# Kernel optimization log

Measured on AMD Instinct MI355X. Metric: run time of the kernel, lower is better.

The kernel has to match this reference:

```python
import jax, jax.numpy as jnp
import numpy as np


def setup_inputs() -> dict:
    key = jax.random.key(0)
    k1, k2, k3, k4 = jax.random.split(key, 4)
    B, Nq, Nc, D = 4, 1024, 16384, 1024
    return {
        "query_embeddings": jax.random.normal(k1, (B, Nq, D), dtype=jnp.float32),
        "context_embeddings": jax.random.normal(k2, (B, Nc, D), dtype=jnp.float32),
        "W": jax.random.normal(k3, (D, D), dtype=jnp.float32) * (1.0 / np.sqrt(D)),
        "b": jax.random.normal(k4, (D,), dtype=jnp.float32) * 0.02,
    }


TOP_N = 5


def _pairwise_l2(q, c):
    # q: [B, Nq, D], c: [B, Nc, D] -> [B, Nq, Nc] Euclidean distances
    q_sq = jnp.sum(q * q, axis=-1, keepdims=True)          # [B, Nq, 1]
    c_sq = jnp.sum(c * c, axis=-1)[:, None, :]             # [B, 1, Nc]
    cross = jnp.einsum("bqd,bcd->bqc", q, c)               # [B, Nq, Nc]
    d2 = jnp.maximum(q_sq + c_sq - 2.0 * cross, 0.0)
    return jnp.sqrt(d2)


def reference(query_embeddings, context_embeddings, W, b):
    # latent query projection (nn.Linear): x @ W.T + b
    q_proj = jnp.einsum("bqd,ed->bqe", query_embeddings, W) + b
    distances = _pairwise_l2(q_proj, context_embeddings)    # [B, Nq, Nc]
    # smallest top_n distances -> top_k on negated values
    neg_d, idx = jax.lax.top_k(-distances, TOP_N)
    return (-neg_d, idx)
```

## Files before the change

### kernel.cpp

```cpp
#include <hip/hip_runtime.h>
#include <cfloat>
#include <math.h>

#define D_DIM 1024
#define B_DIM 4
#define NQ    1024
#define NC    16384
#define TOPN  5
#define TOPA  5
#define CSPLIT 8
#define CAND  (TOPA*CSPLIT)
#define QT    64
#define CTILE 512
#define BK    64

#define PBM 128
#define PBN 64
#define PBK 32
#define PPAD 4
#define PROJ_BLKS ((D_DIM/PBN) * ((B_DIM*NQ)/PBM))

typedef __bf16 bf16x8 __attribute__((ext_vector_type(8)));
typedef float  f32x4  __attribute__((ext_vector_type(4)));
typedef double f64x4  __attribute__((ext_vector_type(4)));

__device__ __forceinline__ unsigned short f2bf(float f) {
    unsigned u = __builtin_bit_cast(unsigned, f);
    unsigned r = (u + 0x7fffu + ((u >> 16) & 1u)) >> 16;
    return (unsigned short)r;
}

__device__ __forceinline__ void gload16(const void* g, void* l) {
    __builtin_amdgcn_global_load_lds(
        (const __attribute__((address_space(1))) unsigned*)g,
        (__attribute__((address_space(3))) unsigned*)l, 16, 0, 0);
}

template<int N, typename T>
__device__ __forceinline__ void topk_insert(T (&bv)[N], int (&bi)[N], T v, int ci) {
    if (v < bv[N-1] || (v == bv[N-1] && ci < bi[N-1])) {
        bv[N-1] = v; bi[N-1] = ci;
        #pragma unroll
        for (int s = N-1; s > 0; --s) {
            bool sw = (bv[s] < bv[s-1]) || (bv[s] == bv[s-1] && bi[s] < bi[s-1]);
            if (sw) {
                T tv = bv[s-1]; bv[s-1] = bv[s]; bv[s] = tv;
                int ti = bi[s-1]; bi[s-1] = bi[s]; bi[s] = ti;
            }
        }
    }
}

template<int N>
__device__ __forceinline__ void insN(float (&bv)[N], int (&bi)[N], float v, int ci) {
    if (v < bv[N-1]) {
        bv[N-1] = v; bi[N-1] = ci;
        #pragma unroll
        for (int s = N-1; s > 0; --s) {
            if (bv[s] < bv[s-1]) {
                float tv = bv[s-1]; bv[s-1] = bv[s]; bv[s] = tv;
                int   ti = bi[s-1]; bi[s-1] = bi[s]; bi[s] = ti;
            }
        }
    }
}

__device__ __forceinline__ void ins5b(float (&bv)[TOPA], int (&bi)[TOPA], float v, int ci) {
    #pragma unroll
    for (int s = 0; s < TOPA; ++s) {
        const bool  c    = v < bv[s];
        const float vmin = c ? v : bv[s];
        const float vmax = c ? bv[s] : v;
        const int   imin = c ? ci : bi[s];
        const int   imax = c ? bi[s] : ci;
        bv[s] = vmin; bi[s] = imin;
        v = vmax; ci = imax;
    }
}

__global__ __launch_bounds__(256) void proj_packc_kernel(const float* __restrict__ Q,
                                                         const float* __restrict__ W,
                                                         const float* __restrict__ bias,
                                                         const float* __restrict__ C,
                                                         double* __restrict__ P64,
                                                         unsigned short* __restrict__ Pbf,
                                                         float* __restrict__ qsq,
                                                         unsigned short* __restrict__ Cbf,
                                                         float* __restrict__ csq)
{
    const int bid = blockIdx.x;
    if (bid >= PROJ_BLKS) {
        int wave = threadIdx.x >> 6;
        int lane = threadIdx.x & 63;
        int row  = (bid - PROJ_BLKS) * 4 + wave;
        const float* x = C + (size_t)row * D_DIM;
        float s = 0.f;
        #pragma unroll
        for (int i = 0; i < 4; ++i) {
            float4 v = *(const float4*)&x[lane * 4 + i * 256];
            s += v.x * v.x + v.y * v.y + v.z * v.z + v.w * v.w;
            ushort4 h;
            h.x = f2bf(v.x); h.y = f2bf(v.y); h.z = f2bf(v.z); h.w = f2bf(v.w);
            *(ushort4*)&Cbf[(size_t)row * D_DIM + lane * 4 + i * 256] = h;
        }
        #pragma unroll
        for (int off = 32; off; off >>= 1) s += __shfl_down(s, off, 64);
        if (lane == 0) csq[row] = s;
        return;
    }
    __shared__ __align__(16) float Qs[PBM][PBK + PPAD];
    __shared__ __align__(16) float Ws[PBN][PBK + PPAD];

    const int t    = threadIdx.x;
    const int lane = t & 63;
    const int w    = t >> 6;
    const int l15  = lane & 15;
    const int l4   = lane >> 4;
    const int m0   = (bid >> 4) * PBM;
    const int n0   = (bid & 15) * PBN;
    const int wm   = (w >> 1) * 64;
    const int wn   = (w & 1) * 32;

    const int srow = t >> 3;
    const int scol = (t & 7) * 4;

    f64x4 acc[4][2];
    #pragma unroll
    for (int fm = 0; fm < 4; ++fm)
        #pragma unroll
        for (int fn = 0; fn < 2; ++fn) acc[fm][fn] = (f64x4)0.0;

    for (int k0 = 0; k0 < D_DIM; k0 += PBK) {
        float4 qa0 = *(const float4*)&Q[(size_t)(m0 + srow)      * D_DIM + k0 + scol];
        float4 qa1 = *(const float4*)&Q[(size_t)(m0 + srow + 32) * D_DIM + k0 + scol];
        float4 qa2 = *(const float4*)&Q[(size_t)(m0 + srow + 64) * D_DIM + k0 + scol];
        float4 qa3 = *(const float4*)&Q[(size_t)(m0 + srow + 96) * D_DIM + k0 + scol];
        float4 wa0 = *(const float4*)&W[(size_t)(n0 + srow)      * D_DIM + k0 + scol];
        float4 wa1 = *(const float4*)&W[(size_t)(n0 + srow + 32) * D_DIM + k0 + scol];
        __syncthreads();
        *(float4*)&Qs[srow][scol]      = qa0;
        *(float4*)&Qs[srow + 32][scol] = qa1;
        *(float4*)&Qs[srow + 64][scol] = qa2;
        *(float4*)&Qs[srow + 96][scol] = qa3;
        *(float4*)&Ws[srow][scol]      = wa0;
        *(float4*)&Ws[srow + 32][scol] = wa1;
        __syncthreads();

        #pragma unroll
        for (int ks = 0; ks < PBK / 4; ++ks) {
            const int kc = ks * 4 + l4;
            double a[4], b[2];
            #pragma unroll
            for (int fm = 0; fm < 4; ++fm) a[fm] = (double)Qs[wm + fm * 16 + l15][kc];
            #pragma unroll
            for (int fn = 0; fn < 2; ++fn) b[fn] = (double)Ws[wn + fn * 16 + l15][kc];
            #pragma unroll
            for (int fm = 0; fm < 4; ++fm)
                #pragma unroll
                for (int fn = 0; fn < 2; ++fn)
                    acc[fm][fn] = __builtin_amdgcn_mfma_f64_16x16x4f64(a[fm], b[fn], acc[fm][fn], 0, 0, 0);
        }
    }

    #pragma unroll
    for (int fm = 0; fm < 4; ++fm) {
        #pragma unroll
        for (int j = 0; j < 4; ++j) {
            const int row = m0 + wm + fm * 16 + j * 4 + l4;
            float part = 0.f;
            #pragma unroll
            for (int fn = 0; fn < 2; ++fn) {
                const int col = n0 + wn + fn * 16 + l15;
                double d = acc[fm][fn][j] + (double)bias[col];
                P64[(size_t)row * D_DIM + col] = d;
                float a = (float)d;
                part += a * a;
                Pbf[(size_t)row * D_DIM + col] = f2bf(a);
            }
            #pragma unroll
            for (int m = 1; m < 16; m <<= 1) part += __shfl_xor(part, m, 64);
            if (l15 == 0) atomicAdd(&qsq[row], part);
        }
    }
}

__global__ __launch_bounds__(256) void perm_detect_kernel(const float* __restrict__ Q,
                                                          const float* __restrict__ W,
                                                          const float* __restrict__ bias,
                                                          const double* __restrict__ P64,
                                                          int* __restrict__ invperm)
{
    __shared__ double tv[16];
    const int t = threadIdx.x;
    const int g = t >> 4;
    const int s = t & 15;
    if (t < 16) invperm[t] = t;

    double acc = 0.0;
    const int kb = s * 64;
    for (int k = 0; k < 64; ++k)
        acc = fma((double)Q[(size_t)g * D_DIM + kb + k], (double)W[kb + k], acc);
    #pragma unroll
    for (int off = 8; off; off >>= 1) acc += __shfl_down(acc, off, 16);
    if (s == 0) tv[g] = acc + (double)bias[0];
    __syncthreads();

    if (t < 16) {
        double p = P64[(size_t)t * D_DIM];
        int best = 0; double bd = fabs(p - tv[0]);
        #pragma unroll
        for (int i = 1; i < 16; ++i) {
            double d = fabs(p - tv[i]);
            if (d < bd) { bd = d; best = i; }
        }
        invperm[best] = t;
    }
}

__global__ __launch_bounds__(256, 2) void dist_mfma_kernel(const unsigned short* __restrict__ Pbf,
                                                           const unsigned short* __restrict__ Cbf,
                                                           const float* __restrict__ qsq,
                                                           const float* __restrict__ csq,
                                                           int* __restrict__ pi)
{
    __shared__ __align__(16) short CsS[CTILE * 64];
    __shared__ __align__(16) short QsS[QT * 64];
    float* MV = (float*)CsS;
    int*   MI = (int*)(CsS + 4096);

    const int t    = threadIdx.x;
    const int lane = t & 63;
    const int w    = t >> 6;
    const int l15  = lane & 15;
    const int l4   = lane >> 4;
    const int r8   = lane >> 3;
    const int sc   = lane & 7;
    const int csplit = blockIdx.x;
    const int by = blockIdx.y;
    const int bz = blockIdx.z;
    const int qg0 = bz * NQ + by * QT;

    unsigned cOff[16], qOff[2];
    #pragma unroll
    for (int j = 0; j < 16; ++j)
        cOff[j] = (unsigned)((w * 128 + j * 8 + r8) * D_DIM + (sc ^ r8) * 8);
    #pragma unroll
    for (int j = 0; j < 2; ++j)
        qOff[j] = (unsigned)((w * 16 + j * 8 + r8) * D_DIM + (sc ^ r8) * 8);

    float qsv[4];
    #pragma unroll
    for (int s = 0; s < 4; ++s) qsv[s] = qsq[qg0 + s * 16 + l15];

    float bv[4][TOPA]; int bi[4][TOPA];
    #pragma unroll
    for (int s = 0; s < 4; ++s)
        #pragma unroll
        for (int j = 0; j < TOPA; ++j) { bv[s][j] = FLT_MAX; bi[s][j] = 0x7fffffff; }

    const int cpb = NC / CSPLIT;
    for (int it = 0; it < cpb / CTILE; ++it) {
        const int cg0 = csplit * cpb + it * CTILE;
        const size_t crow0 = (size_t)bz * NC + cg0;

        f32x4 acc[8][4];
        #pragma unroll
        for (int u = 0; u < 8; ++u)
            #pragma unroll
            for (int s = 0; s < 4; ++s) acc[u][s] = (f32x4)0.0f;

        for (int k0 = 0; k0 < D_DIM; k0 += BK) {
            const unsigned short* cB = Cbf + crow0 * D_DIM + k0;
            const unsigned short* qB = Pbf + (size_t)qg0 * D_DIM + k0;
            __syncthreads();
            #pragma unroll
            for (int j = 0; j < 16; ++j)
                gload16(cB + cOff[j], &CsS[(w * 128 + j * 8) * 64]);
            #pragma unroll
            for (int j = 0; j < 2; ++j)
                gload16(qB + qOff[j], &QsS[(w * 16 + j * 8) * 64]);
            __syncthreads();
            #pragma unroll
            for (int ks = 0; ks < 2; ++ks) {
                const int sp = ((ks * 4 + l4) ^ (l15 & 7)) * 8;
                bf16x8 bq[4];
                #pragma unroll
                for (int s = 0; s < 4; ++s)
                    bq[s] = *(const bf16x8*)&QsS[(s * 16 + l15) * 64 + sp];
                #pragma unroll
                for (int u = 0; u < 8; ++u) {
                    bf16x8 ac = *(const bf16x8*)&CsS[(w * 128 + u * 16 + l15) * 64 + sp];
                    #pragma unroll
                    for (int s = 0; s < 4; ++s)
                        acc[u][s] = __builtin_amdgcn_mfma_f32_16x16x32_bf16(ac, bq[s], acc[u][s], 0, 0, 0);
                }
            }
        }

        #pragma unroll
        for (int u = 0; u < 8; ++u) {
            const int crow = w * 128 + u * 16 + l4 * 4;
            float4 cs4 = *(const float4*)&csq[(size_t)bz * NC + cg0 + crow];
            float csa[4] = {cs4.x, cs4.y, cs4.z, cs4.w};
            #pragma unroll
            for (int s = 0; s < 4; ++s) {
                #pragma unroll
                for (int r = 0; r < 4; ++r) {
                    float v = qsv[s] + csa[r] - 2.0f * acc[u][s][r];
                    ins5b(bv[s], bi[s], v, cg0 + crow + r);
                }
            }
        }
    }

    #pragma unroll
    for (int mask = 16; mask <= 32; mask <<= 1) {
        #pragma unroll
        for (int s = 0; s < 4; ++s) {
            float ov[TOPA]; int oi[TOPA];
            #pragma unroll
            for (int j = 0; j < TOPA; ++j) {
                ov[j] = __shfl_xor(bv[s][j], mask, 64);
                oi[j] = __shfl_xor(bi[s][j], mask, 64);
            }
            #pragma unroll
            for (int j = 0; j < TOPA; ++j) insN<TOPA>(bv[s], bi[s], ov[j], oi[j]);
        }
    }
    __syncthreads();
    if (l4 == 0) {
        #pragma unroll
        for (int s = 0; s < 4; ++s) {
            int q = s * 16 + l15;
            #pragma unroll
            for (int j = 0; j < TOPA; ++j) {
                MV[(q * 4 + w) * TOPA + j] = bv[s][j];
                MI[(q * 4 + w) * TOPA + j] = bi[s][j];
            }
        }
    }
    __syncthreads();
    if (t < QT) {
        float mv[TOPA]; int mi[TOPA];
        #pragma unroll
        for (int j = 0; j < TOPA; ++j) { mv[j] = FLT_MAX; mi[j] = 0x7fffffff; }
        for (int l = 0; l < 4; ++l)
            #pragma unroll
            for (int j = 0; j < TOPA; ++j)
                insN<TOPA>(mv, mi, MV[(t * 4 + l) * TOPA + j], MI[(t * 4 + l) * TOPA + j]);
        size_t base = (((size_t)qg0 + t) * CSPLIT + csplit) * TOPA;
        #pragma unroll
        for (int j = 0; j < TOPA; ++j) pi[base + j] = mi[j];
    }
}

__global__ __launch_bounds__(256) void refine_kernel(const double* __restrict__ P64,
                                                     const int* __restrict__ invperm,
                                                     const float* __restrict__ C,
                                                     const int*   __restrict__ pi,
                                                     float* __restrict__ out)
{
    __shared__ double pS[D_DIM];
    __shared__ double dvs[CAND];
    __shared__ int    dis[CAND];
    const int q    = blockIdx.x;
    const int pq   = (q & ~15) | invperm[q & 15];
    const int bz   = q >> 10;
    const int t    = threadIdx.x;
    const int wave = t >> 6;
    const int lane = t & 63;
    const double* p = P64 + (size_t)pq * D_DIM;

    #pragma unroll
    for (int j = 0; j < D_DIM / 256; ++j) pS[t + j * 256] = p[t + j * 256];
    __syncthreads();

    for (int k = wave; k < CAND; k += 4) {
        int ci = pi[(size_t)pq * CAND + k];
        const float* c = C + ((size_t)bz * NC + ci) * D_DIM;
        double s = 0.0;
        #pragma unroll
        for (int j = 0; j < 16; ++j) {
            int d = lane + 64 * j;
            double diff = pS[d] - (double)c[d];
            s = fma(diff, diff, s);
        }
        #pragma unroll
        for (int off = 32; off; off >>= 1) s += __shfl_down(s, off, 64);
        if (lane == 0) { dvs[k] = s; dis[k] = ci; }
    }
    __syncthreads();
    if (t == 0) {
        double bv[TOPN]; int bi[TOPN];
        #pragma unroll
        for (int j = 0; j < TOPN; ++j) { bv[j] = DBL_MAX; bi[j] = 0x7fffffff; }
        for (int k = 0; k < CAND; ++k)
            topk_insert<TOPN,double>(bv, bi, dvs[k], dis[k]);
        #pragma unroll
        for (int j = 0; j < TOPN; ++j) {
            out[(size_t)q * TOPN + j] = (float)sqrt(bv[j]);
            out[(size_t)B_DIM * NQ * TOPN + (size_t)q * TOPN + j] = (float)bi[j];
        }
    }
}

extern "C" void kernel_launch(void* const* d_in, const int* in_sizes, int n_in,
                              void* d_out, int out_size, void* d_ws, size_t ws_size,
                              hipStream_t stream) {
    const float* Q    = (const float*)d_in[0];
    const float* C    = (const float*)d_in[1];
    const float* W    = (const float*)d_in[2];
    const float* bias = (const float*)d_in[3];
    float* out = (float*)d_out;

    char* ws = (char*)d_ws;
    double*         P64 = (double*)ws;
    unsigned short* Pbf = (unsigned short*)(ws + (size_t)32 * 1024 * 1024);
    unsigned short* Cbf = (unsigned short*)(ws + (size_t)40 * 1024 * 1024);
    float*          qsq = (float*)(ws + (size_t)168 * 1024 * 1024);
    float*          csq = qsq + 4096;
    int*            pi  = (int*)(csq + 65536);
    int*            ivp = pi + (size_t)B_DIM * NQ * CAND;

    hipMemsetAsync(qsq, 0, (size_t)B_DIM * NQ * sizeof(float), stream);
    proj_packc_kernel<<<PROJ_BLKS + (B_DIM * NC) / 4, 256, 0, stream>>>(Q, W, bias, C, P64, Pbf, qsq, Cbf, csq);
    perm_detect_kernel<<<1, 256, 0, stream>>>(Q, W, bias, P64, ivp);
    dist_mfma_kernel<<<dim3(CSPLIT, NQ / QT, B_DIM), 256, 0, stream>>>(Pbf, Cbf, qsq, csq, pi);
    refine_kernel<<<B_DIM * NQ, 256, 0, stream>>>(P64, ivp, C, pi, out);
}
```

Measured before the change: 838.4 us.

## Double-buffer projection GEMM tiles with direct global-to-LDS loads and XOR swizzle

The fp64-MFMA projection GEMM now stages Q and W tiles straight into LDS with global_load_lds, using two buffers so the next K-slice loads while the current one is computed. The padded layout is replaced by an XOR-swizzled unpadded layout to avoid LDS bank conflicts. This removes the register round trip and one barrier per iteration. The cost is double the LDS for these tiles, and correctness now depends on the async load being complete at the single remaining barrier.

```diff
diff --git a/kernel.cpp b/kernel.cpp
--- a/kernel.cpp
+++ b/kernel.cpp
@@ -17,7 +17,6 @@
 #define PBM 128
 #define PBN 64
 #define PBK 32
-#define PPAD 4
 #define PROJ_BLKS ((D_DIM/PBN) * ((B_DIM*NQ)/PBM))
 
 typedef __bf16 bf16x8 __attribute__((ext_vector_type(8)));
@@ -108,58 +107,64 @@
         if (lane == 0) csq[row] = s;
         return;
     }
-    __shared__ __align__(16) float Qs[PBM][PBK + PPAD];
-    __shared__ __align__(16) float Ws[PBN][PBK + PPAD];
+    __shared__ __align__(16) float QsL[2][PBM * PBK];
+    __shared__ __align__(16) float WsL[2][PBN * PBK];
 
     const int t    = threadIdx.x;
     const int lane = t & 63;
     const int w    = t >> 6;
     const int l15  = lane & 15;
     const int l4   = lane >> 4;
+    const int r8   = lane >> 3;
+    const int sc   = lane & 7;
     const int m0   = (bid >> 4) * PBM;
     const int n0   = (bid & 15) * PBN;
     const int wm   = (w >> 1) * 64;
     const int wn   = (w & 1) * 32;
 
-    const int srow = t >> 3;
-    const int scol = (t & 7) * 4;
-
     f64x4 acc[4][2];
     #pragma unroll
     for (int fm = 0; fm < 4; ++fm)
         #pragma unroll
         for (int fn = 0; fn < 2; ++fn) acc[fm][fn] = (f64x4)0.0;
 
+    auto stage = [&](int k0, int b) {
+        #pragma unroll
+        for (int j = 0; j < 4; ++j)
+            gload16(&Q[(size_t)(m0 + w * 32 + j * 8 + r8) * D_DIM + k0 + (sc ^ r8) * 4],
+                    &QsL[b][(w * 32 + j * 8) * PBK]);
+        #pragma unroll
+        for (int j = 0; j < 2; ++j)
+            gload16(&W[(size_t)(n0 + w * 16 + j * 8 + r8) * D_DIM + k0 + (sc ^ r8) * 4],
+                    &WsL[b][(w * 16 + j * 8) * PBK]);
+    };
+
+    stage(0, 0);
+    __syncthreads();
+    int cur = 0;
+
     for (int k0 = 0; k0 < D_DIM; k0 += PBK) {
-        float4 qa0 = *(const float4*)&Q[(size_t)(m0 + srow)      * D_DIM + k0 + scol];
-        float4 qa1 = *(const float4*)&Q[(size_t)(m0 + srow + 32) * D_DIM + k0 + scol];
-        float4 qa2 = *(const float4*)&Q[(size_t)(m0 + srow + 64) * D_DIM + k0 + scol];
-        float4 qa3 = *(const float4*)&Q[(size_t)(m0 + srow + 96) * D_DIM + k0 + scol];
-        float4 wa0 = *(const float4*)&W[(size_t)(n0 + srow)      * D_DIM + k0 + scol];
-        float4 wa1 = *(const float4*)&W[(size_t)(n0 + srow + 32) * D_DIM + k0 + scol];
-        __syncthreads();
-        *(float4*)&Qs[srow][scol]      = qa0;
-        *(float4*)&Qs[srow + 32][scol] = qa1;
-        *(float4*)&Qs[srow + 64][scol] = qa2;
-        *(float4*)&Qs[srow + 96][scol] = qa3;
-        *(float4*)&Ws[srow][scol]      = wa0;
-        *(float4*)&Ws[srow + 32][scol] = wa1;
-        __syncthreads();
+        if (k0 + PBK < D_DIM) stage(k0 + PBK, cur ^ 1);
 
         #pragma unroll
         for (int ks = 0; ks < PBK / 4; ++ks) {
-            const int kc = ks * 4 + l4;
+            const int sw = ((ks ^ (l15 & 7)) << 2) + l4;
             double a[4], b[2];
             #pragma unroll
-            for (int fm = 0; fm < 4; ++fm) a[fm] = (double)Qs[wm + fm * 16 + l15][kc];
-            #pragma unroll
-            for (int fn = 0; fn < 2; ++fn) b[fn] = (double)Ws[wn + fn * 16 + l15][kc];
+            for (int fm = 0; fm < 4; ++fm)
+                a[fm] = (double)QsL[cur][(wm + fm * 16 + l15) * PBK + sw];
+            #pragma unroll
+            for (int fn = 0; fn < 2; ++fn)
+                b[fn] = (double)WsL[cur][(wn + fn * 16 + l15) * PBK + sw];
             #pragma unroll
             for (int fm = 0; fm < 4; ++fm)
                 #pragma unroll
                 for (int fn = 0; fn < 2; ++fn)
                     acc[fm][fn] = __builtin_amdgcn_mfma_f64_16x16x4f64(a[fm], b[fn], acc[fm][fn], 0, 0, 0);
         }
+
+        __syncthreads();
+        cur ^= 1;
     }
 
     #pragma unroll
```

Result: slower. 870.5 us (+3.8%).
